# Optimization experiments

Hardware: AMD Instinct MI355X
Metric: run time of the kernel (lower is better)

Reference implementation:

```python
import jax, jax.numpy as jnp
import numpy as np

B, L, C = 4, 2048, 1024
H = 16
D = C // H  # 64
MAX_SCALE_MUL = float(np.log(100.0))


def setup_inputs() -> dict:
    key = jax.random.key(0)
    ks = jax.random.split(key, 8)
    x = jax.random.normal(ks[0], (B, L, C), dtype=jnp.float32)
    attn_bias = jax.random.normal(ks[1], (1, H, L, L), dtype=jnp.float32) * 0.02
    # nn.Linear(C, 3C, bias=False): weight [3C, C], init ~ U(-1/sqrt(C), 1/sqrt(C))
    lim = 1.0 / np.sqrt(C)
    W_qkv = jax.random.uniform(ks[2], (3 * C, C), minval=-lim, maxval=lim, dtype=jnp.float32)
    q_bias = jnp.zeros((C,), dtype=jnp.float32)
    v_bias = jnp.zeros((C,), dtype=jnp.float32)
    scale_mul_log = jnp.full((1, H, 1, 1), np.log(4.0), dtype=jnp.float32)
    W_proj = jax.random.uniform(ks[3], (C, C), minval=-lim, maxval=lim, dtype=jnp.float32)
    b_proj = jax.random.uniform(ks[4], (C,), minval=-lim, maxval=lim, dtype=jnp.float32)
    return {"x": x, "attn_bias": attn_bias, "W_qkv": W_qkv, "q_bias": q_bias,
            "v_bias": v_bias, "scale_mul_log": scale_mul_log,
            "W_proj": W_proj, "b_proj": b_proj}


def reference(x, attn_bias, W_qkv, q_bias, v_bias, scale_mul_log, W_proj, b_proj):
    Bc, Lc, Cc = x.shape
    qkv_bias = jnp.concatenate([q_bias, jnp.zeros_like(q_bias), v_bias])
    qkv = x @ W_qkv.T + qkv_bias                      # [B, L, 3C]
    qkv = qkv.reshape(Bc, Lc, 3, H, D)
    q, k, v = jnp.moveaxis(qkv, 2, 0)                 # each [B, L, H, D]
    q = jnp.swapaxes(q, 1, 2)                         # [B, H, L, D]
    k = jnp.swapaxes(k, 1, 2)
    v = jnp.swapaxes(v, 1, 2)
    # L2-norm cosine attention with learned per-head scale
    scale_mul = jnp.exp(jnp.minimum(scale_mul_log, MAX_SCALE_MUL))  # [1, H, 1, 1]
    q = q / jnp.linalg.norm(q, axis=-1, keepdims=True).clip(1e-12) * scale_mul
    k = k / jnp.linalg.norm(k, axis=-1, keepdims=True).clip(1e-12)
    attn = jnp.einsum('bhqd,bhkd->bhqk', q, k) + attn_bias
    attn = jax.nn.softmax(attn, axis=-1)
    out = jnp.einsum('bhqk,bhkd->bhqd', attn, v)      # [B, H, L, D]
    out = jnp.swapaxes(out, 1, 2).reshape(Bc, Lc, Cc)
    return out @ W_proj.T + b_proj
```

## Files before the change

kernel.cpp:

```cpp
#include <hip/hip_runtime.h>
#include <cstdint>
#include <cstddef>

#define BATCH 4
#define SEQ   2048
#define CMOD  1024
#define NH    16
#define DH    64
#define LOG100 4.6051701859880914f
#define LOG2E  1.4426950408889634f

typedef __attribute__((ext_vector_type(8))) short bf16x8;
typedef __attribute__((ext_vector_type(4))) float f32x4;
typedef __attribute__((ext_vector_type(16))) float f32x16;

__device__ __forceinline__ float u32lo_f(uint32_t u) {
    union { uint32_t i; float f; } x; x.i = u << 16; return x.f;
}
__device__ __forceinline__ float u32hi_f(uint32_t u) {
    union { uint32_t i; float f; } x; x.i = u & 0xFFFF0000u; return x.f;
}
__device__ __forceinline__ uint16_t f2bf(float f) {
    union { float f; uint32_t i; } x; x.f = f;
    uint32_t u = x.i;
    return (uint16_t)((u + 0x7FFFu + ((u >> 16) & 1u)) >> 16);
}
__device__ __forceinline__ float exp2_fast(float x) {
    float r; asm("v_exp_f32 %0, %1" : "=v"(r) : "v"(x)); return r;
}
__device__ __forceinline__ uint32_t cvt_pk_bf16(float lo, float hi) {
    uint32_t r;
    asm("v_cvt_pk_bf16_f32 %0, %1, %2" : "=v"(r) : "v"(lo), "v"(hi));
    return r;
}
__device__ __forceinline__ void p32swap(uint32_t& x, uint32_t& y) {
#if __has_builtin(__builtin_amdgcn_permlane32_swap)
    auto r = __builtin_amdgcn_permlane32_swap(x, y, false, false);
    x = r[0]; y = r[1];
#else
    asm volatile("v_permlane32_swap_b32 %0, %1\n\ts_nop 1" : "+v"(x), "+v"(y));
#endif
}

__device__ __forceinline__ void gload_lds16(const void* g, void* l) {
    __builtin_amdgcn_global_load_lds(
        (const __attribute__((address_space(1))) uint32_t*)g,
        (__attribute__((address_space(3))) uint32_t*)l,
        16, 0, 0);
}

__global__ __launch_bounds__(256) void cvt_kernel(const float* __restrict__ in,
                                                  uint16_t* __restrict__ out, int n) {
    int i = (blockIdx.x * 256 + threadIdx.x) * 4;
    if (i >= n) return;
    float4 f = *(const float4*)(in + i);
    ushort4 o;
    o.x = f2bf(f.x); o.y = f2bf(f.y); o.z = f2bf(f.z); o.w = f2bf(f.w);
    *(ushort4*)(out + i) = o;
}

__global__ __launch_bounds__(256) void gemm_bt_kernel(
    const uint16_t* __restrict__ A, const uint16_t* __restrict__ B,
    int M, int N, int K, int mode,
    uint16_t* __restrict__ qb, uint16_t* __restrict__ kb, uint16_t* __restrict__ vtb,
    const float* __restrict__ q_bias, const float* __restrict__ v_bias,
    const float* __restrict__ scale_mul_log,
    float* __restrict__ outp, const float* __restrict__ b_proj)
{
    __shared__ __align__(16) uint16_t As[128 * 32];
    __shared__ __align__(16) uint16_t Bs[128 * 32];
    const int t = threadIdx.x;
    const int wave = t >> 6, lane = t & 63;
    const int g = lane >> 4, c16 = lane & 15;
    const int m0 = blockIdx.x * 128, n0 = blockIdx.y * 128;
    const int wm = (wave >> 1) * 64, wn = (wave & 1) * 64;

    f32x4 acc[4][4];
#pragma unroll
    for (int mt = 0; mt < 4; mt++)
#pragma unroll
        for (int nt = 0; nt < 4; nt++) acc[mt][nt] = (f32x4){0.f, 0.f, 0.f, 0.f};

    for (int k0 = 0; k0 < K; k0 += 32) {
        __syncthreads();
#pragma unroll
        for (int i = 0; i < 2; i++) {
            int cc = i * 256 + t;
            int row = cc >> 2, col = (cc & 3) * 8;
            gload_lds16(A + (size_t)(m0 + row) * K + k0 + col, &As[cc * 8]);
            gload_lds16(B + (size_t)(n0 + row) * K + k0 + col, &Bs[cc * 8]);
        }
        __syncthreads();
        bf16x8 af[4], bfv[4];
#pragma unroll
        for (int mt = 0; mt < 4; mt++)
            af[mt] = *(const bf16x8*)&As[(wm + mt * 16 + c16) * 32 + g * 8];
#pragma unroll
        for (int nt = 0; nt < 4; nt++)
            bfv[nt] = *(const bf16x8*)&Bs[(wn + nt * 16 + c16) * 32 + g * 8];
#pragma unroll
        for (int mt = 0; mt < 4; mt++)
#pragma unroll
            for (int nt = 0; nt < 4; nt++)
                acc[mt][nt] = __builtin_amdgcn_mfma_f32_16x16x32_bf16(af[mt], bfv[nt], acc[mt][nt], 0, 0, 0);
    }

    if (mode == 0) {
        const int colbase = n0 + wn;
        const int tt = colbase >> 10;
        const int cc0 = colbase & 1023;
        const int hh = cc0 >> 6;
        float qmul = 1.0f;
        if (tt == 0) qmul = __expf(fminf(scale_mul_log[hh], LOG100)) * LOG2E;
#pragma unroll
        for (int mt = 0; mt < 4; mt++) {
            float vals[4][4];
            float n2[4] = {0.f, 0.f, 0.f, 0.f};
#pragma unroll
            for (int nt = 0; nt < 4; nt++) {
                const int ci = cc0 + nt * 16 + c16;
                float badd = 0.f;
                if (tt == 0) badd = q_bias[ci];
                else if (tt == 2) badd = v_bias[ci];
#pragma unroll
                for (int r = 0; r < 4; r++) {
                    float v = acc[mt][nt][r] + badd;
                    vals[nt][r] = v;
                    n2[r] += v * v;
                }
            }
            float rs[4];
            if (tt < 2) {
#pragma unroll
                for (int r = 0; r < 4; r++) {
                    float s = n2[r];
                    s += __shfl_xor(s, 1, 64);
                    s += __shfl_xor(s, 2, 64);
                    s += __shfl_xor(s, 4, 64);
                    s += __shfl_xor(s, 8, 64);
                    rs[r] = qmul / fmaxf(sqrtf(s), 1e-12f);
                }
            } else {
#pragma unroll
                for (int r = 0; r < 4; r++) rs[r] = 1.0f;
            }
#pragma unroll
            for (int nt = 0; nt < 4; nt++) {
                const int dd = (cc0 + nt * 16 + c16) & 63;
#pragma unroll
                for (int r = 0; r < 4; r++) {
                    const int row = m0 + wm + mt * 16 + g * 4 + r;
                    const int bb = row >> 11, ll = row & 2047;
                    const size_t bhx = (size_t)bb * NH + hh;
                    const uint16_t val = f2bf(vals[nt][r] * rs[r]);
                    if (tt < 2) {
                        size_t addr = ((bhx * 64 + (ll >> 5)) * 4 + (dd >> 4)) * 512
                                      + ((dd >> 3) & 1) * 256 + (ll & 31) * 8 + (dd & 7);
                        if (tt == 0) qb[addr] = val; else kb[addr] = val;
                    } else {
                        size_t addr = ((bhx * 64 + (ll >> 5)) * 4 + (dd >> 5) * 2 + ((ll >> 4) & 1)) * 512
                                      + (((ll >> 3) & 1) * 32 + (dd & 31)) * 8 + (ll & 7);
                        vtb[addr] = val;
                    }
                }
            }
        }
    } else {
#pragma unroll
        for (int mt = 0; mt < 4; mt++)
#pragma unroll
            for (int nt = 0; nt < 4; nt++)
#pragma unroll
                for (int r = 0; r < 4; r++) {
                    int row = m0 + wm + mt * 16 + g * 4 + r;
                    int col = n0 + wn + nt * 16 + c16;
                    outp[(size_t)row * N + col] = acc[mt][nt][r] + b_proj[col];
                }
    }
}

__global__ __launch_bounds__(256) void attn_kernel(
    const uint16_t* __restrict__ qfrag, const uint16_t* __restrict__ kfrag,
    const uint16_t* __restrict__ vfrag, const float* __restrict__ bias,
    uint16_t* __restrict__ ob)
{
    __shared__ __align__(16) uint16_t KsL[2 * 4 * 4 * 512];
    __shared__ __align__(16) uint16_t VsL[2 * 4 * 4 * 512];
    __shared__ __align__(16) uint2    Bsh[2 * 8 * 64];

    const int t = threadIdx.x;
    const int w = t >> 6, lane = t & 63;
    const int c32 = lane & 31, hi = lane >> 5;

    const int h = blockIdx.x >> 5;
    const int qt = blockIdx.x & 31;
    const int q0 = qt * 64;
    const size_t bh = (size_t)w * NH + h;

    bf16x8 qf[2][4];
#pragma unroll
    for (int qg = 0; qg < 2; qg++)
#pragma unroll
        for (int s = 0; s < 4; s++)
            qf[qg][s] = *(const bf16x8*)(qfrag +
                ((bh * 64 + (size_t)(qt * 2 + qg)) * 4 + s) * 512 + hi * 256 + c32 * 8);

    auto stage = [&](int tl, int buf) {
        const uint16_t* kp = kfrag + ((bh * 64 + (size_t)tl) * 4) * 512 + lane * 8;
        const uint16_t* vp = vfrag + ((bh * 64 + (size_t)tl) * 4) * 512 + lane * 8;
#pragma unroll
        for (int s = 0; s < 4; s++)
            gload_lds16(kp + s * 512, &KsL[((buf * 4 + w) * 4 + s) * 512 + lane * 8]);
#pragma unroll
        for (int s = 0; s < 4; s++)
            gload_lds16(vp + s * 512, &VsL[((buf * 4 + w) * 4 + s) * 512 + lane * 8]);
    };

    f32x16 accO[2][2];
#pragma unroll
    for (int qg = 0; qg < 2; qg++)
#pragma unroll
        for (int db = 0; db < 2; db++)
#pragma unroll
            for (int i = 0; i < 16; i++) accO[qg][db][i] = 0.f;
    float lrun[2] = {0.f, 0.f};

    const int brow = t >> 2, g0 = (t & 3) * 2;
    const float* bgl = bias + ((size_t)h * SEQ + q0 + brow) * SEQ + (t & 3) * 8;

    float4 br0 = *(const float4*)(bgl);
    float4 br1 = *(const float4*)(bgl + 4);
    stage(0, 0);
    asm volatile("s_waitcnt vmcnt(0)" ::: "memory");
    Bsh[g0 * 64 + brow] = make_uint2(cvt_pk_bf16(br0.x * LOG2E, br0.y * LOG2E),
                                     cvt_pk_bf16(br0.z * LOG2E, br0.w * LOG2E));
    Bsh[(g0 + 1) * 64 + brow] = make_uint2(cvt_pk_bf16(br1.x * LOG2E, br1.y * LOG2E),
                                           cvt_pk_bf16(br1.z * LOG2E, br1.w * LOG2E));
    br0 = *(const float4*)(bgl + 32);
    br1 = *(const float4*)(bgl + 36);
    __syncthreads();

    for (int it = 0; it < 64; ++it) {
        const int cur = it & 1;
        if (it < 63) {
            const int nb = cur ^ 1;
            Bsh[nb * 512 + g0 * 64 + brow] =
                make_uint2(cvt_pk_bf16(br0.x * LOG2E, br0.y * LOG2E),
                           cvt_pk_bf16(br0.z * LOG2E, br0.w * LOG2E));
            Bsh[nb * 512 + (g0 + 1) * 64 + brow] =
                make_uint2(cvt_pk_bf16(br1.x * LOG2E, br1.y * LOG2E),
                           cvt_pk_bf16(br1.z * LOG2E, br1.w * LOG2E));
            int nt2 = it + 2; if (nt2 > 63) nt2 = 63;
            br0 = *(const float4*)(bgl + nt2 * 32);
            br1 = *(const float4*)(bgl + nt2 * 32 + 4);
            stage(it + 1, nb);
        }

        bf16x8 kf[4], vf[4];
#pragma unroll
        for (int s = 0; s < 4; s++)
            kf[s] = *(const bf16x8*)&KsL[((cur * 4 + w) * 4 + s) * 512 + lane * 8];
#pragma unroll
        for (int s = 0; s < 4; s++)
            vf[s] = *(const bf16x8*)&VsL[((cur * 4 + w) * 4 + s) * 512 + lane * 8];

#pragma unroll
        for (int qg = 0; qg < 2; qg++) {
            f32x16 S;
#pragma unroll
            for (int i = 0; i < 16; i++) S[i] = 0.f;
#pragma unroll
            for (int s = 0; s < 4; s++)
                S = __builtin_amdgcn_mfma_f32_32x32x16_bf16(kf[s], qf[qg][s], S, 0, 0, 0);

            float p[16];
            float lp = 0.f;
#pragma unroll
            for (int tt = 0; tt < 4; tt++) {
                uint2 uu = Bsh[cur * 512 + (tt * 2 + hi) * 64 + qg * 32 + c32];
                p[tt * 4 + 0] = exp2_fast(S[tt * 4 + 0] + u32lo_f(uu.x));
                p[tt * 4 + 1] = exp2_fast(S[tt * 4 + 1] + u32hi_f(uu.x));
                p[tt * 4 + 2] = exp2_fast(S[tt * 4 + 2] + u32lo_f(uu.y));
                p[tt * 4 + 3] = exp2_fast(S[tt * 4 + 3] + u32hi_f(uu.y));
                lp += (p[tt * 4 + 0] + p[tt * 4 + 1]) + (p[tt * 4 + 2] + p[tt * 4 + 3]);
            }
            lrun[qg] += lp;

            bf16x8 pa[2];
#pragma unroll
            for (int cp = 0; cp < 2; cp++) {
                uint32_t X0 = cvt_pk_bf16(p[8 * cp + 0], p[8 * cp + 1]);
                uint32_t X1 = cvt_pk_bf16(p[8 * cp + 2], p[8 * cp + 3]);
                uint32_t Y0 = cvt_pk_bf16(p[8 * cp + 4], p[8 * cp + 5]);
                uint32_t Y1 = cvt_pk_bf16(p[8 * cp + 6], p[8 * cp + 7]);
                p32swap(X0, Y0);
                p32swap(X1, Y1);
                union { uint32_t u[4]; bf16x8 v; } pu;
                pu.u[0] = X0; pu.u[1] = X1; pu.u[2] = Y0; pu.u[3] = Y1;
                pa[cp] = pu.v;
            }

#pragma unroll
            for (int c = 0; c < 2; c++)
#pragma unroll
                for (int db = 0; db < 2; db++)
                    accO[qg][db] = __builtin_amdgcn_mfma_f32_32x32x16_bf16(
                        pa[c], vf[db * 2 + c], accO[qg][db], 0, 0, 0);
        }

        __syncthreads();
    }

#pragma unroll
    for (int qg = 0; qg < 2; qg++) {
        float s = lrun[qg] + __shfl_xor(lrun[qg], 32, 64);
        float inv = 1.0f / s;
        float linv[16];
#pragma unroll
        for (int r = 0; r < 16; r++)
            linv[r] = __shfl(inv, (r & 3) + 8 * (r >> 2) + 4 * hi, 64);
#pragma unroll
        for (int r = 0; r < 16; r++) {
            int rowq = (r & 3) + 8 * (r >> 2) + 4 * hi;
            size_t rowbase = ((size_t)w * SEQ + q0 + qg * 32 + rowq) * CMOD + h * DH;
            ob[rowbase + c32]      = f2bf(accO[qg][0][r] * linv[r]);
            ob[rowbase + 32 + c32] = f2bf(accO[qg][1][r] * linv[r]);
        }
    }
}

extern "C" void kernel_launch(void* const* d_in, const int* in_sizes, int n_in,
                              void* d_out, int out_size, void* d_ws, size_t ws_size,
                              hipStream_t stream) {
    const float* x             = (const float*)d_in[0];
    const float* attn_bias     = (const float*)d_in[1];
    const float* W_qkv         = (const float*)d_in[2];
    const float* q_bias        = (const float*)d_in[3];
    const float* v_bias        = (const float*)d_in[4];
    const float* scale_mul_log = (const float*)d_in[5];
    const float* W_proj        = (const float*)d_in[6];
    const float* b_proj        = (const float*)d_in[7];
    float* out = (float*)d_out;

    uint8_t* ws = (uint8_t*)d_ws;
    size_t off = 0;
    auto alloc = [&](size_t bytes) { uint8_t* p = ws + off; off += (bytes + 255) & ~(size_t)255; return p; };
    uint16_t* xb     = (uint16_t*)alloc((size_t)8192 * 1024 * 2);
    uint16_t* wqkvb  = (uint16_t*)alloc((size_t)3072 * 1024 * 2);
    uint16_t* wprojb = (uint16_t*)alloc((size_t)1024 * 1024 * 2);
    uint16_t* qb     = (uint16_t*)alloc((size_t)BATCH * NH * SEQ * DH * 2);
    uint16_t* kb     = (uint16_t*)alloc((size_t)BATCH * NH * SEQ * DH * 2);
    uint16_t* vtb    = (uint16_t*)alloc((size_t)BATCH * NH * SEQ * DH * 2);
    uint16_t* ob     = (uint16_t*)alloc((size_t)BATCH * SEQ * CMOD * 2);
    (void)ws_size;

    cvt_kernel<<<8192, 256, 0, stream>>>(x, xb, 8388608);
    cvt_kernel<<<3072, 256, 0, stream>>>(W_qkv, wqkvb, 3145728);
    cvt_kernel<<<1024, 256, 0, stream>>>(W_proj, wprojb, 1048576);

    dim3 g1(64, 24);
    gemm_bt_kernel<<<g1, 256, 0, stream>>>(xb, wqkvb, 8192, 3072, 1024, 0,
                                           qb, kb, vtb, q_bias, v_bias, scale_mul_log,
                                           nullptr, nullptr);

    attn_kernel<<<512, 256, 0, stream>>>(qb, kb, vtb, attn_bias, ob);

    dim3 g3(64, 8);
    gemm_bt_kernel<<<g3, 256, 0, stream>>>(ob, wprojb, 8192, 1024, 1024, 1,
                                           nullptr, nullptr, nullptr, nullptr, nullptr, nullptr,
                                           out, b_proj);
}
```

Before: 296.2 us.

## Use partial vmcnt waits and priority hints to overlap attention tile loads

Replaces the full __syncthreads and vmcnt(0) waits with counted waits (vmcnt(10)) and lgkmcnt plus raw s_barrier, so the next K/V tile and bias loads stay in flight while the current tile computes. It also reorders the bias LDS layout so the two halves of each wave read contiguous entries, and wraps the MFMA groups in s_setprio to favour matrix issue. The risk is correctness if the vmcnt count does not match the number of outstanding loads for the current buffer.

```diff
diff --git a/kernel.cpp b/kernel.cpp
--- a/kernel.cpp
+++ b/kernel.cpp
@@ -186,7 +186,7 @@
 {
     __shared__ __align__(16) uint16_t KsL[2 * 4 * 4 * 512];
     __shared__ __align__(16) uint16_t VsL[2 * 4 * 4 * 512];
-    __shared__ __align__(16) uint2    Bsh[2 * 8 * 64];
+    __shared__ __align__(16) uint2    Bsh[2 * 512];
 
     const int t = threadIdx.x;
     const int w = t >> 6, lane = t & 63;
@@ -216,6 +216,19 @@
             gload_lds16(vp + s * 512, &VsL[((buf * 4 + w) * 4 + s) * 512 + lane * 8]);
     };
 
+    const int brow = t >> 2, kpart = t & 3;
+    const float* bgl = bias + ((size_t)h * SEQ + q0 + brow) * SEQ + kpart * 8;
+    const int u0 = kpart * 128 + (brow >> 5) * 64 + (brow & 31);
+
+    auto writeBsh = [&](int buf, float4 a, float4 b) {
+        Bsh[buf * 512 + u0] =
+            make_uint2(cvt_pk_bf16(a.x * LOG2E, a.y * LOG2E),
+                       cvt_pk_bf16(a.z * LOG2E, a.w * LOG2E));
+        Bsh[buf * 512 + u0 + 32] =
+            make_uint2(cvt_pk_bf16(b.x * LOG2E, b.y * LOG2E),
+                       cvt_pk_bf16(b.z * LOG2E, b.w * LOG2E));
+    };
+
     f32x16 accO[2][2];
 #pragma unroll
     for (int qg = 0; qg < 2; qg++)
@@ -225,35 +238,31 @@
             for (int i = 0; i < 16; i++) accO[qg][db][i] = 0.f;
     float lrun[2] = {0.f, 0.f};
 
-    const int brow = t >> 2, g0 = (t & 3) * 2;
-    const float* bgl = bias + ((size_t)h * SEQ + q0 + brow) * SEQ + (t & 3) * 8;
-
-    float4 br0 = *(const float4*)(bgl);
-    float4 br1 = *(const float4*)(bgl + 4);
+    float4 a0 = *(const float4*)(bgl);
+    float4 a1 = *(const float4*)(bgl + 4);
+    float4 br0 = *(const float4*)(bgl + 32);
+    float4 br1 = *(const float4*)(bgl + 36);
+    __builtin_amdgcn_sched_barrier(0);
     stage(0, 0);
-    asm volatile("s_waitcnt vmcnt(0)" ::: "memory");
-    Bsh[g0 * 64 + brow] = make_uint2(cvt_pk_bf16(br0.x * LOG2E, br0.y * LOG2E),
-                                     cvt_pk_bf16(br0.z * LOG2E, br0.w * LOG2E));
-    Bsh[(g0 + 1) * 64 + brow] = make_uint2(cvt_pk_bf16(br1.x * LOG2E, br1.y * LOG2E),
-                                           cvt_pk_bf16(br1.z * LOG2E, br1.w * LOG2E));
-    br0 = *(const float4*)(bgl + 32);
-    br1 = *(const float4*)(bgl + 36);
-    __syncthreads();
+    writeBsh(0, a0, a1);
+    asm volatile("s_waitcnt lgkmcnt(0)" ::: "memory");
+    __builtin_amdgcn_s_barrier();
 
     for (int it = 0; it < 64; ++it) {
         const int cur = it & 1;
         if (it < 63) {
             const int nb = cur ^ 1;
-            Bsh[nb * 512 + g0 * 64 + brow] =
-                make_uint2(cvt_pk_bf16(br0.x * LOG2E, br0.y * LOG2E),
-                           cvt_pk_bf16(br0.z * LOG2E, br0.w * LOG2E));
-            Bsh[nb * 512 + (g0 + 1) * 64 + brow] =
-                make_uint2(cvt_pk_bf16(br1.x * LOG2E, br1.y * LOG2E),
-                           cvt_pk_bf16(br1.z * LOG2E, br1.w * LOG2E));
-            int nt2 = it + 2; if (nt2 > 63) nt2 = 63;
-            br0 = *(const float4*)(bgl + nt2 * 32);
-            br1 = *(const float4*)(bgl + nt2 * 32 + 4);
+            writeBsh(nb, br0, br1);
+            int n2 = it + 2; if (n2 > 63) n2 = 63;
+            br0 = *(const float4*)(bgl + n2 * 32);
+            br1 = *(const float4*)(bgl + n2 * 32 + 4);
+            __builtin_amdgcn_sched_barrier(0);
             stage(it + 1, nb);
+            asm volatile("s_waitcnt vmcnt(10)" ::: "memory");
+            __builtin_amdgcn_sched_barrier(0);
+        } else {
+            asm volatile("s_waitcnt vmcnt(0)" ::: "memory");
+            __builtin_amdgcn_sched_barrier(0);
         }
 
         bf16x8 kf[4], vf[4];
@@ -269,15 +278,17 @@
             f32x16 S;
 #pragma unroll
             for (int i = 0; i < 16; i++) S[i] = 0.f;
+            __builtin_amdgcn_s_setprio(1);
 #pragma unroll
             for (int s = 0; s < 4; s++)
                 S = __builtin_amdgcn_mfma_f32_32x32x16_bf16(kf[s], qf[qg][s], S, 0, 0, 0);
+            __builtin_amdgcn_s_setprio(0);
 
             float p[16];
             float lp = 0.f;
 #pragma unroll
             for (int tt = 0; tt < 4; tt++) {
-                uint2 uu = Bsh[cur * 512 + (tt * 2 + hi) * 64 + qg * 32 + c32];
+                uint2 uu = Bsh[cur * 512 + tt * 128 + qg * 64 + hi * 32 + c32];
                 p[tt * 4 + 0] = exp2_fast(S[tt * 4 + 0] + u32lo_f(uu.x));
                 p[tt * 4 + 1] = exp2_fast(S[tt * 4 + 1] + u32hi_f(uu.x));
                 p[tt * 4 + 2] = exp2_fast(S[tt * 4 + 2] + u32lo_f(uu.y));
@@ -300,15 +311,18 @@
                 pa[cp] = pu.v;
             }
 
+            __builtin_amdgcn_s_setprio(1);
 #pragma unroll
             for (int c = 0; c < 2; c++)
 #pragma unroll
                 for (int db = 0; db < 2; db++)
                     accO[qg][db] = __builtin_amdgcn_mfma_f32_32x32x16_bf16(
                         pa[c], vf[db * 2 + c], accO[qg][db], 0, 0, 0);
-        }
-
-        __syncthreads();
+            __builtin_amdgcn_s_setprio(0);
+        }
+
+        asm volatile("s_waitcnt lgkmcnt(0)" ::: "memory");
+        __builtin_amdgcn_s_barrier();
     }
 
 #pragma unroll
```

After: 323.6 us. 1.09x slower.
